# Kernel optimization log

Measured on AMD Instinct MI355X. Metric: run time of the kernel, lower is better.

## Reference

```python
import jax, jax.numpy as jnp
import numpy as np

N_NODES = 50000
N_EDGES = 800000
IN_FEATS = 128
HIDDEN = 128
OUT_LEN = 128


def setup_inputs() -> dict:
    key = jax.random.key(0)
    ks = jax.random.split(key, 8)
    feat = jax.random.normal(ks[0], (N_NODES, IN_FEATS), dtype=jnp.float32)
    # Glorot-ish init for weights, zeros for bias (DGL GraphConv default)
    def w(k, fi, fo):
        return jax.random.normal(k, (fi, fo), dtype=jnp.float32) / np.sqrt(fi)
    W1 = w(ks[1], IN_FEATS, HIDDEN)
    W2 = w(ks[2], HIDDEN, HIDDEN)
    W3 = w(ks[3], HIDDEN, OUT_LEN)
    b1 = jnp.zeros((HIDDEN,), jnp.float32)
    b2 = jnp.zeros((HIDDEN,), jnp.float32)
    b3 = jnp.zeros((OUT_LEN,), jnp.float32)
    src = jax.random.randint(ks[4], (N_EDGES,), 0, N_NODES, dtype=jnp.int32)
    dst = jax.random.randint(ks[5], (N_EDGES,), 0, N_NODES, dtype=jnp.int32)
    return {"feat": feat, "W1": W1, "b1": b1, "W2": W2, "b2": b2,
            "W3": W3, "b3": b3, "src": src, "dst": dst}


def _degree_norm(idx, n):
    # degree counts, clamped to min 1 (DGL behavior), then ^{-1/2}
    deg = jax.ops.segment_sum(jnp.ones_like(idx, dtype=jnp.float32), idx,
                              num_segments=n)
    return jax.lax.rsqrt(jnp.maximum(deg, 1.0))


def _graph_conv(x, W, b, src, dst, out_norm, in_norm):
    # DGL GraphConv, norm='both':
    # h = D_dst^{-1/2} * segsum_dst( D_src^{-1/2} * x[src] ) @ W + b
    h = x * out_norm[:, None]
    m = jax.ops.segment_sum(h[src], dst, num_segments=x.shape[0])  # [N, d]
    m = m * in_norm[:, None]
    return m @ W + b


def reference(feat, W1, b1, W2, b2, W3, b3, src, dst):
    out_norm = _degree_norm(src, feat.shape[0])  # out-degree norm (source)
    in_norm = _degree_norm(dst, feat.shape[0])   # in-degree norm (dest)
    h = jax.nn.relu(_graph_conv(feat, W1, b1, src, dst, out_norm, in_norm))
    h = jax.nn.relu(_graph_conv(h, W2, b2, src, dst, out_norm, in_norm))
    h = _graph_conv(h, W3, b3, src, dst, out_norm, in_norm)
    # single graph: mean_nodes == mean over all nodes, then squeeze -> [out_len]
    return jnp.mean(h, axis=0)
```

## Files before the change

### kernel.cpp

```cpp
#include <hip/hip_runtime.h>

#define N_NODES 50000
#define N_EDGES 800000
#define F 128
#define SCAN_NB 49
#define CH 64
#define EPC (N_EDGES / CH)
#define HALF 25000
#define QTR 12500
#define BSTRIDE 17
#define AGG_NB (N_NODES / 4)
#define RED_NB 256

typedef __bf16 bf16x8 __attribute__((ext_vector_type(8)));
typedef float  f32x4  __attribute__((ext_vector_type(4)));
typedef float  f32x2  __attribute__((ext_vector_type(2)));

__device__ inline unsigned short f2bf(float f) {
    unsigned u = __float_as_uint(f);
    u += 0x7FFF + ((u >> 16) & 1);
    return (unsigned short)(u >> 16);
}
__device__ inline unsigned packbf2(float a, float b) {
    return (unsigned)f2bf(a) | ((unsigned)f2bf(b) << 16);
}

__device__ inline void fp8x8_to_f32(uint2 u, float* f) {
    f32x2 v0 = __builtin_amdgcn_cvt_pk_f32_fp8(u.x, false);
    f32x2 v1 = __builtin_amdgcn_cvt_pk_f32_fp8(u.x, true);
    f32x2 v2 = __builtin_amdgcn_cvt_pk_f32_fp8(u.y, false);
    f32x2 v3 = __builtin_amdgcn_cvt_pk_f32_fp8(u.y, true);
    f[0] = v0.x; f[1] = v0.y; f[2] = v1.x; f[3] = v1.y;
    f[4] = v2.x; f[5] = v2.y; f[6] = v3.x; f[7] = v3.y;
}
__device__ inline unsigned f32x4_to_fp8(float a, float b, float c, float d) {
    unsigned r = __builtin_amdgcn_cvt_pk_fp8_f32(a, b, 0, false);
    r = __builtin_amdgcn_cvt_pk_fp8_f32(c, d, r, true);
    return r;
}

__global__ __launch_bounds__(1024) void hist_kernel(const int* __restrict__ src,
                                                    const int* __restrict__ dst,
                                                    unsigned short* __restrict__ Hs16,
                                                    unsigned short* __restrict__ Hd16) {
    __shared__ unsigned hist[HALF / 2];
    int bx = blockIdx.x;
    int c = bx >> 2, t = bx & 1, h = (bx >> 1) & 1;
    const int* ids = t ? dst : src;
    unsigned short* H = t ? Hd16 : Hs16;
    int base = h * HALF;
    for (int j = threadIdx.x; j < HALF / 2; j += 1024) hist[j] = 0;
    __syncthreads();
    int e0 = c * EPC;
    for (int e = e0 + threadIdx.x; e < e0 + EPC; e += 1024) {
        int id = ids[e] - base;
        if ((unsigned)id < (unsigned)HALF)
            atomicAdd(&hist[id >> 1], 1u << ((id & 1) * 16));
    }
    __syncthreads();
    for (int j = threadIdx.x; j < HALF / 2; j += 1024)
        *(unsigned*)&H[(size_t)c * N_NODES + base + 2 * j] = hist[j];
}

__global__ __launch_bounds__(1024) void reduceN_kernel(const unsigned short* __restrict__ Hs16,
                                                       const unsigned short* __restrict__ Hd16,
                                                       float* __restrict__ onorm,
                                                       float* __restrict__ inorm,
                                                       int* __restrict__ degd,
                                                       int* __restrict__ bsums) {
    __shared__ int wsum[16];
    int i = blockIdx.x * 1024 + threadIdx.x;
    int dd = 0;
    if (i < N_NODES) {
        int ds = 0;
        for (int c = 0; c < CH; c++) {
            ds += Hs16[(size_t)c * N_NODES + i];
            dd += Hd16[(size_t)c * N_NODES + i];
        }
        onorm[i] = rsqrtf(fmaxf((float)ds, 1.0f));
        inorm[i] = rsqrtf(fmaxf((float)dd, 1.0f));
        degd[i] = dd;
    }
    int v = dd;
#pragma unroll
    for (int off = 32; off; off >>= 1) v += __shfl_down(v, off);
    if ((threadIdx.x & 63) == 0) wsum[threadIdx.x >> 6] = v;
    __syncthreads();
    if (threadIdx.x == 0) {
        int s = 0;
#pragma unroll
        for (int k = 0; k < 16; k++) s += wsum[k];
        bsums[blockIdx.x] = s;
    }
}

__global__ __launch_bounds__(64) void scanB_kernel(const int* __restrict__ blockSums,
                                                   int* __restrict__ blockOffs) {
    int t = threadIdx.x;
    int v = (t < SCAN_NB) ? blockSums[t] : 0;
    int incl = v;
#pragma unroll
    for (int off = 1; off < 64; off <<= 1) {
        int u = __shfl_up(incl, off);
        if (t >= off) incl += u;
    }
    if (t < SCAN_NB) blockOffs[t] = incl - v;
}

__global__ __launch_bounds__(1024) void tq_kernel(const int* __restrict__ src,
                                                  const int* __restrict__ dst,
                                                  const float* __restrict__ inorm,
                                                  float* __restrict__ Tq) {
    __shared__ float a[QTR];
    int bx = blockIdx.x;
    int c = bx >> 2, q = bx & 3;
    int base = q * QTR;
    for (int j = threadIdx.x; j < QTR; j += 1024) a[j] = 0.0f;
    __syncthreads();
    int e0 = c * EPC;
    for (int e = e0 + threadIdx.x; e < e0 + EPC; e += 1024) {
        int s = src[e] - base;
        if ((unsigned)s < (unsigned)QTR)
            atomicAdd(&a[s], inorm[dst[e]]);
    }
    __syncthreads();
    for (int j = threadIdx.x; j < QTR; j += 1024)
        Tq[(size_t)c * N_NODES + base + j] = a[j];
}

__global__ __launch_bounds__(1024) void scanC_kernel(const int* __restrict__ deg,
                                                     const int* __restrict__ blockOffs,
                                                     int* __restrict__ rowst,
                                                     const unsigned short* __restrict__ Hd16,
                                                     int* __restrict__ P,
                                                     const float* __restrict__ Tq,
                                                     float* __restrict__ qt) {
    __shared__ int wsum[16];
    int t = threadIdx.x, lane = t & 63, w = t >> 6;
    int i = blockIdx.x * 1024 + t;
    int v = (i < N_NODES) ? deg[i] : 0;
    int incl = v;
#pragma unroll
    for (int off = 1; off < 64; off <<= 1) {
        int u = __shfl_up(incl, off);
        if (lane >= off) incl += u;
    }
    if (lane == 63) wsum[w] = incl;
    __syncthreads();
    if (t == 0) {
        int s = 0;
#pragma unroll
        for (int k = 0; k < 16; k++) { int x = wsum[k]; wsum[k] = s; s += x; }
    }
    __syncthreads();
    incl += wsum[w] + blockOffs[blockIdx.x];
    if (i < N_NODES) {
        int s = incl - v;
        rowst[i] = s;
        if (i == N_NODES - 1) rowst[N_NODES] = incl;
        float tsum = 0.0f;
        for (int c = 0; c < CH; c++) {
            size_t o = (size_t)c * N_NODES + i;
            P[o] = s; s += Hd16[o];
            tsum += Tq[o];
        }
        qt[i] = tsum;
    }
}

__global__ __launch_bounds__(1024) void scatter2_kernel(const int* __restrict__ src,
                                                        const int* __restrict__ dst,
                                                        const int* __restrict__ P,
                                                        int* __restrict__ esrc) {
    __shared__ int cur[QTR];
    int bx = blockIdx.x;
    int c = bx >> 2, q = bx & 3;
    int base = q * QTR;
    for (int j = threadIdx.x; j < QTR; j += 1024)
        cur[j] = P[(size_t)c * N_NODES + base + j];
    __syncthreads();
    int e0 = c * EPC;
    for (int e = e0 + threadIdx.x; e < e0 + EPC; e += 1024) {
        int d = dst[e] - base;
        if ((unsigned)d < (unsigned)QTR) {
            int pos = atomicAdd(&cur[d], 1);
            esrc[pos] = src[e];
        }
    }
}

__global__ __launch_bounds__(256) void cvt_kernel(const float* __restrict__ x,
                                                  const float* __restrict__ onorm,
                                                  uint2* __restrict__ xq, int n8) {
    int i = blockIdx.x * 256 + threadIdx.x;
    if (i < n8) {
        float w = onorm[i >> 4];
        const float4* xv = (const float4*)x;
        float4 v0 = xv[i * 2], v1 = xv[i * 2 + 1];
        uint2 o;
        o.x = f32x4_to_fp8(v0.x * w, v0.y * w, v0.z * w, v0.w * w);
        o.y = f32x4_to_fp8(v1.x * w, v1.y * w, v1.z * w, v1.w * w);
        xq[i] = o;
    }
}

__global__ __launch_bounds__(128) void wprep_kernel(const float* __restrict__ W1,
                                                    const float* __restrict__ W2,
                                                    unsigned short* __restrict__ Wt_hi,
                                                    unsigned short* __restrict__ Wt_lo) {
    int bx = blockIdx.x;
    int wi = bx >> 7, n = bx & 127;
    const float* W = wi ? W2 : W1;
    int k = threadIdx.x;
    float v = W[k * F + n];
    unsigned short hi = f2bf(v);
    float r = v - __uint_as_float((unsigned)hi << 16);
    size_t o = (size_t)wi * F * F + (size_t)n * F + k;
    Wt_hi[o] = hi;
    Wt_lo[o] = f2bf(r);
}

__global__ __launch_bounds__(256) void agg_csr_kernel(const uint2* __restrict__ xq,
                                                      uint4* __restrict__ mb,
                                                      const int* __restrict__ rowst,
                                                      const int* __restrict__ esrc,
                                                      const float* __restrict__ inorm) {
    int w = threadIdx.x >> 6;
    int lane = threadIdx.x & 63;
    int g = lane >> 4, t = lane & 15;
    int row = blockIdx.x * 4 + w;
    int beg = __builtin_amdgcn_readfirstlane(rowst[row]);
    int end = __builtin_amdgcn_readfirstlane(rowst[row + 1]);
    float acc[8];
#pragma unroll
    for (int k = 0; k < 8; k++) acc[k] = 0.0f;

    for (int e = beg; e < end; e += 16) {
        int ea = min(e + g,      end - 1);
        int eb = min(e + 4 + g,  end - 1);
        int ec = min(e + 8 + g,  end - 1);
        int ed = min(e + 12 + g, end - 1);
        int sa = esrc[ea], sb = esrc[eb], sc = esrc[ec], sd = esrc[ed];
        uint2 ua = xq[(size_t)sa * 16 + t];
        uint2 ub = xq[(size_t)sb * 16 + t];
        uint2 uc = xq[(size_t)sc * 16 + t];
        uint2 ud = xq[(size_t)sd * 16 + t];
        float wa = (e + g      < end) ? 1.0f : 0.0f;
        float wb = (e + 4 + g  < end) ? 1.0f : 0.0f;
        float wc = (e + 8 + g  < end) ? 1.0f : 0.0f;
        float wd = (e + 12 + g < end) ? 1.0f : 0.0f;
        float fa[8], fb[8], fc[8], fd[8];
        fp8x8_to_f32(ua, fa); fp8x8_to_f32(ub, fb);
        fp8x8_to_f32(uc, fc); fp8x8_to_f32(ud, fd);
#pragma unroll
        for (int k = 0; k < 8; k++)
            acc[k] += fa[k] * wa + fb[k] * wb + fc[k] * wc + fd[k] * wd;
    }
#pragma unroll
    for (int k = 0; k < 8; k++) {
        acc[k] += __shfl_xor(acc[k], 16, 64);
        acc[k] += __shfl_xor(acc[k], 32, 64);
    }
    if (g == 0) {
        float inw = inorm[row];
        uint4 o;
        o.x = packbf2(acc[0] * inw, acc[1] * inw);
        o.y = packbf2(acc[2] * inw, acc[3] * inw);
        o.z = packbf2(acc[4] * inw, acc[5] * inw);
        o.w = packbf2(acc[6] * inw, acc[7] * inw);
        mb[(size_t)row * 16 + t] = o;
    }
}

__global__ __launch_bounds__(256) void mfma_gemm_kernel(const unsigned short* __restrict__ A,
                                                        const unsigned short* __restrict__ Wt_hi,
                                                        const unsigned short* __restrict__ Wt_lo,
                                                        const float* __restrict__ bias,
                                                        const float* __restrict__ onorm,
                                                        unsigned char* __restrict__ Y8) {
    __shared__ uint4 sB[F * BSTRIDE];
    int tid = threadIdx.x;
    int w = tid >> 6;
    int lane = tid & 63;
    int quad = lane >> 4, r16 = lane & 15;
    int row0 = blockIdx.x * 64 + w * 16;

    const uint4* Arow = (const uint4*)(A + (size_t)(row0 + r16) * F);
    uint4 a[4];
#pragma unroll
    for (int kk = 0; kk < 4; kk++) a[kk] = Arow[kk * 4 + quad];

    f32x4 acc[8];
#pragma unroll
    for (int t = 0; t < 8; t++) acc[t] = (f32x4){0.f, 0.f, 0.f, 0.f};

    const uint4* G[2] = {(const uint4*)Wt_hi, (const uint4*)Wt_lo};
#pragma unroll
    for (int ph = 0; ph < 2; ph++) {
        if (ph) __syncthreads();
        for (int j = tid; j < F * 16; j += 256)
            sB[(j >> 4) * BSTRIDE + (j & 15)] = G[ph][j];
        __syncthreads();
#pragma unroll
        for (int kk = 0; kk < 4; kk++) {
            bf16x8 av = __builtin_bit_cast(bf16x8, a[kk]);
#pragma unroll
            for (int t = 0; t < 8; t++) {
                bf16x8 bv = __builtin_bit_cast(bf16x8,
                    sB[(t * 16 + r16) * BSTRIDE + kk * 4 + quad]);
                acc[t] = __builtin_amdgcn_mfma_f32_16x16x32_bf16(av, bv, acc[t], 0, 0, 0);
            }
        }
    }

    float onw[4];
#pragma unroll
    for (int reg = 0; reg < 4; reg++) {
        int row = row0 + quad * 4 + reg;
        onw[reg] = (row < N_NODES) ? onorm[row] : 0.0f;
    }
#pragma unroll
    for (int t = 0; t < 8; t++) {
        int col = t * 16 + r16;
        float bb = bias[col];
#pragma unroll
        for (int reg = 0; reg < 4; reg++) {
            int row = row0 + quad * 4 + reg;
            if (row < N_NODES) {
                float v = fmaxf(acc[t][reg] + bb, 0.0f) * onw[reg];
                unsigned p = __builtin_amdgcn_cvt_pk_fp8_f32(v, v, 0, false);
                Y8[(size_t)row * F + col] = (unsigned char)(p & 0xFF);
            }
        }
    }
}

__global__ __launch_bounds__(256) void colsum_kernel(const unsigned short* __restrict__ x8,
                                                     const float* __restrict__ qt,
                                                     float* __restrict__ part2) {
    __shared__ float sP[4][F];
    int tid = threadIdx.x;
    int w = tid >> 6, lane = tid & 63;
    float a0 = 0.0f, a1 = 0.0f;
    for (int r = blockIdx.x * 4 + w; r < N_NODES; r += RED_NB * 4) {
        float q = qt[r];
        unsigned us = x8[(size_t)r * 64 + lane];
        f32x2 v = __builtin_amdgcn_cvt_pk_f32_fp8(us, false);
        a0 += v.x * q; a1 += v.y * q;
    }
    sP[w][lane * 2] = a0; sP[w][lane * 2 + 1] = a1;
    __syncthreads();
    if (tid < F)
        part2[(size_t)blockIdx.x * F + tid] =
            sP[0][tid] + sP[1][tid] + sP[2][tid] + sP[3][tid];
}

__global__ __launch_bounds__(1024) void final_kernel(const float* __restrict__ part2,
                                                     const float* __restrict__ W3,
                                                     const float* __restrict__ b3,
                                                     float* __restrict__ out) {
    __shared__ float sc[8][F];
    int tid = threadIdx.x;
    int col = tid & 127, sl = tid >> 7;
    float acc = 0.0f;
    for (int b = sl; b < RED_NB; b += 8) acc += part2[(size_t)b * F + col];
    sc[sl][col] = acc;
    __syncthreads();
    if (tid < F) {
        float s = 0.0f;
#pragma unroll
        for (int k = 0; k < 8; k++) s += sc[k][tid];
        sc[0][tid] = s * (1.0f / (float)N_NODES);
    }
    __syncthreads();
    if (tid < F) {
        float o = b3[tid];
        for (int k = 0; k < F; k++) o += sc[0][k] * W3[k * F + tid];
        out[tid] = o;
    }
}

extern "C" void kernel_launch(void* const* d_in, const int* in_sizes, int n_in,
                              void* d_out, int out_size, void* d_ws, size_t ws_size,
                              hipStream_t stream) {
    const float* feat = (const float*)d_in[0];
    const float* W1   = (const float*)d_in[1];
    const float* b1   = (const float*)d_in[2];
    const float* W2   = (const float*)d_in[3];
    const float* b2   = (const float*)d_in[4];
    const float* W3   = (const float*)d_in[5];
    const float* b3   = (const float*)d_in[6];
    const int*   src  = (const int*)d_in[7];
    const int*   dst  = (const int*)d_in[8];
    float* out = (float*)d_out;

    char* ws = (char*)d_ws;
    size_t off = 0;
    uint4* mb    = (uint4*)(ws + off); off += (size_t)N_NODES * F * 2;
    float* Tq    = (float*)(ws + off); off += (size_t)CH * N_NODES * 4;
    int*   P     = (int*)  (ws + off); off += (size_t)CH * N_NODES * 4;
    unsigned short* Hs16 = (unsigned short*)(ws + off); off += (size_t)CH * N_NODES * 2;
    unsigned short* Hd16 = (unsigned short*)(ws + off); off += (size_t)CH * N_NODES * 2;
    uint2* xq    = (uint2*)(ws + off); off += (size_t)N_NODES * F;
    uint2* hq    = (uint2*)(ws + off); off += (size_t)N_NODES * F;
    unsigned short* Wt_hi = (unsigned short*)(ws + off); off += 2 * F * F * 2;
    unsigned short* Wt_lo = (unsigned short*)(ws + off); off += 2 * F * F * 2;
    float* part2 = (float*)(ws + off); off += (size_t)RED_NB * F * 4;
    int*   esrc  = (int*)  (ws + off); off += (size_t)N_EDGES * 4;
    float* onorm = (float*)(ws + off); off += N_NODES * 4;
    float* inorm = (float*)(ws + off); off += N_NODES * 4;
    float* qt    = (float*)(ws + off); off += N_NODES * 4;
    int*   degd  = (int*)  (ws + off); off += N_NODES * 4;
    int*   rowst = (int*)  (ws + off); off += (N_NODES + 1) * 4;
    int*   bsums = (int*)  (ws + off); off += 64 * 4;
    int*   boffs = (int*)  (ws + off); off += 64 * 4;

    const int GB = (N_NODES + 63) / 64;

    hist_kernel<<<4 * CH, 1024, 0, stream>>>(src, dst, Hs16, Hd16);
    reduceN_kernel<<<SCAN_NB, 1024, 0, stream>>>(Hs16, Hd16, onorm, inorm, degd, bsums);
    scanB_kernel<<<1, 64, 0, stream>>>(bsums, boffs);
    tq_kernel<<<4 * CH, 1024, 0, stream>>>(src, dst, inorm, Tq);
    scanC_kernel<<<SCAN_NB, 1024, 0, stream>>>(degd, boffs, rowst, Hd16, P, Tq, qt);
    scatter2_kernel<<<4 * CH, 1024, 0, stream>>>(src, dst, P, esrc);

    cvt_kernel<<<(N_NODES * F / 8 + 255) / 256, 256, 0, stream>>>(feat, onorm, xq, N_NODES * F / 8);
    wprep_kernel<<<256, 128, 0, stream>>>(W1, W2, Wt_hi, Wt_lo);

    agg_csr_kernel<<<AGG_NB, 256, 0, stream>>>(xq, mb, rowst, esrc, inorm);
    mfma_gemm_kernel<<<GB, 256, 0, stream>>>((const unsigned short*)mb, Wt_hi, Wt_lo, b1,
                                             onorm, (unsigned char*)hq);
    agg_csr_kernel<<<AGG_NB, 256, 0, stream>>>(hq, mb, rowst, esrc, inorm);
    mfma_gemm_kernel<<<GB, 256, 0, stream>>>((const unsigned short*)mb, Wt_hi + F * F,
                                             Wt_lo + F * F, b2, onorm, (unsigned char*)xq);
    colsum_kernel<<<RED_NB, 256, 0, stream>>>((const unsigned short*)xq, qt, part2);
    final_kernel<<<1, 1024, 0, stream>>>(part2, W3, b3, out);
}
```

Baseline: 245.9 us.

## Merge graph-build stages and epilogue into cooperative kernels with grid syncs

Eight preprocessing launches (histogram, degree reduce, block scan, Tq, row-start scan, scatter, feature conversion, weight prep) are replaced by one cooperative kernel. The stages are now separated by grid.sync, and the small block-offset scan is folded into a serial prefix sum in each block. The colsum and final kernels are likewise merged into one cooperative kernel. This removes launch gaps and inter-kernel bubbles. In exchange it adds grid-wide barrier costs and requires all 256 blocks of 1024 threads with 50KB of shared memory to be co-resident, and the conversion and weight-prep loops now run on fewer threads.

Result: slower. 442.8 us (+80.1%).

```diff
diff --git a/kernel.cpp b/kernel.cpp
--- a/kernel.cpp
+++ b/kernel.cpp
@@ -1,4 +1,7 @@
 #include <hip/hip_runtime.h>
+#include <hip/hip_cooperative_groups.h>
+
+namespace cg = cooperative_groups;
 
 #define N_NODES 50000
 #define N_EDGES 800000
@@ -39,185 +42,162 @@
     return r;
 }
 
-__global__ __launch_bounds__(1024) void hist_kernel(const int* __restrict__ src,
-                                                    const int* __restrict__ dst,
-                                                    unsigned short* __restrict__ Hs16,
-                                                    unsigned short* __restrict__ Hd16) {
-    __shared__ unsigned hist[HALF / 2];
-    int bx = blockIdx.x;
-    int c = bx >> 2, t = bx & 1, h = (bx >> 1) & 1;
-    const int* ids = t ? dst : src;
-    unsigned short* H = t ? Hd16 : Hs16;
-    int base = h * HALF;
-    for (int j = threadIdx.x; j < HALF / 2; j += 1024) hist[j] = 0;
-    __syncthreads();
-    int e0 = c * EPC;
-    for (int e = e0 + threadIdx.x; e < e0 + EPC; e += 1024) {
-        int id = ids[e] - base;
-        if ((unsigned)id < (unsigned)HALF)
-            atomicAdd(&hist[id >> 1], 1u << ((id & 1) * 16));
-    }
-    __syncthreads();
-    for (int j = threadIdx.x; j < HALF / 2; j += 1024)
-        *(unsigned*)&H[(size_t)c * N_NODES + base + 2 * j] = hist[j];
-}
-
-__global__ __launch_bounds__(1024) void reduceN_kernel(const unsigned short* __restrict__ Hs16,
-                                                       const unsigned short* __restrict__ Hd16,
-                                                       float* __restrict__ onorm,
-                                                       float* __restrict__ inorm,
-                                                       int* __restrict__ degd,
-                                                       int* __restrict__ bsums) {
-    __shared__ int wsum[16];
-    int i = blockIdx.x * 1024 + threadIdx.x;
-    int dd = 0;
-    if (i < N_NODES) {
-        int ds = 0;
-        for (int c = 0; c < CH; c++) {
-            ds += Hs16[(size_t)c * N_NODES + i];
-            dd += Hd16[(size_t)c * N_NODES + i];
-        }
-        onorm[i] = rsqrtf(fmaxf((float)ds, 1.0f));
-        inorm[i] = rsqrtf(fmaxf((float)dd, 1.0f));
-        degd[i] = dd;
-    }
-    int v = dd;
-#pragma unroll
-    for (int off = 32; off; off >>= 1) v += __shfl_down(v, off);
-    if ((threadIdx.x & 63) == 0) wsum[threadIdx.x >> 6] = v;
-    __syncthreads();
-    if (threadIdx.x == 0) {
-        int s = 0;
-#pragma unroll
-        for (int k = 0; k < 16; k++) s += wsum[k];
-        bsums[blockIdx.x] = s;
-    }
-}
-
-__global__ __launch_bounds__(64) void scanB_kernel(const int* __restrict__ blockSums,
-                                                   int* __restrict__ blockOffs) {
-    int t = threadIdx.x;
-    int v = (t < SCAN_NB) ? blockSums[t] : 0;
-    int incl = v;
-#pragma unroll
-    for (int off = 1; off < 64; off <<= 1) {
-        int u = __shfl_up(incl, off);
-        if (t >= off) incl += u;
-    }
-    if (t < SCAN_NB) blockOffs[t] = incl - v;
-}
-
-__global__ __launch_bounds__(1024) void tq_kernel(const int* __restrict__ src,
-                                                  const int* __restrict__ dst,
-                                                  const float* __restrict__ inorm,
-                                                  float* __restrict__ Tq) {
-    __shared__ float a[QTR];
-    int bx = blockIdx.x;
-    int c = bx >> 2, q = bx & 3;
-    int base = q * QTR;
-    for (int j = threadIdx.x; j < QTR; j += 1024) a[j] = 0.0f;
-    __syncthreads();
-    int e0 = c * EPC;
-    for (int e = e0 + threadIdx.x; e < e0 + EPC; e += 1024) {
-        int s = src[e] - base;
-        if ((unsigned)s < (unsigned)QTR)
-            atomicAdd(&a[s], inorm[dst[e]]);
-    }
-    __syncthreads();
-    for (int j = threadIdx.x; j < QTR; j += 1024)
-        Tq[(size_t)c * N_NODES + base + j] = a[j];
-}
-
-__global__ __launch_bounds__(1024) void scanC_kernel(const int* __restrict__ deg,
-                                                     const int* __restrict__ blockOffs,
-                                                     int* __restrict__ rowst,
-                                                     const unsigned short* __restrict__ Hd16,
-                                                     int* __restrict__ P,
-                                                     const float* __restrict__ Tq,
-                                                     float* __restrict__ qt) {
-    __shared__ int wsum[16];
-    int t = threadIdx.x, lane = t & 63, w = t >> 6;
-    int i = blockIdx.x * 1024 + t;
-    int v = (i < N_NODES) ? deg[i] : 0;
-    int incl = v;
-#pragma unroll
-    for (int off = 1; off < 64; off <<= 1) {
-        int u = __shfl_up(incl, off);
-        if (lane >= off) incl += u;
-    }
-    if (lane == 63) wsum[w] = incl;
-    __syncthreads();
-    if (t == 0) {
-        int s = 0;
-#pragma unroll
-        for (int k = 0; k < 16; k++) { int x = wsum[k]; wsum[k] = s; s += x; }
-    }
-    __syncthreads();
-    incl += wsum[w] + blockOffs[blockIdx.x];
-    if (i < N_NODES) {
-        int s = incl - v;
-        rowst[i] = s;
-        if (i == N_NODES - 1) rowst[N_NODES] = incl;
-        float tsum = 0.0f;
-        for (int c = 0; c < CH; c++) {
-            size_t o = (size_t)c * N_NODES + i;
-            P[o] = s; s += Hd16[o];
-            tsum += Tq[o];
-        }
-        qt[i] = tsum;
-    }
-}
-
-__global__ __launch_bounds__(1024) void scatter2_kernel(const int* __restrict__ src,
-                                                        const int* __restrict__ dst,
-                                                        const int* __restrict__ P,
-                                                        int* __restrict__ esrc) {
-    __shared__ int cur[QTR];
-    int bx = blockIdx.x;
-    int c = bx >> 2, q = bx & 3;
-    int base = q * QTR;
-    for (int j = threadIdx.x; j < QTR; j += 1024)
-        cur[j] = P[(size_t)c * N_NODES + base + j];
-    __syncthreads();
-    int e0 = c * EPC;
-    for (int e = e0 + threadIdx.x; e < e0 + EPC; e += 1024) {
-        int d = dst[e] - base;
-        if ((unsigned)d < (unsigned)QTR) {
-            int pos = atomicAdd(&cur[d], 1);
-            esrc[pos] = src[e];
-        }
-    }
-}
-
-__global__ __launch_bounds__(256) void cvt_kernel(const float* __restrict__ x,
-                                                  const float* __restrict__ onorm,
-                                                  uint2* __restrict__ xq, int n8) {
-    int i = blockIdx.x * 256 + threadIdx.x;
-    if (i < n8) {
-        float w = onorm[i >> 4];
-        const float4* xv = (const float4*)x;
+__global__ __launch_bounds__(1024) void build_kernel(
+        const int* __restrict__ src, const int* __restrict__ dst,
+        unsigned short* __restrict__ Hs16, unsigned short* __restrict__ Hd16,
+        float* __restrict__ onorm, float* __restrict__ inorm,
+        int* __restrict__ degd, int* __restrict__ bsums,
+        int* __restrict__ rowst, int* __restrict__ P,
+        float* __restrict__ Tq, float* __restrict__ qt,
+        int* __restrict__ esrc,
+        const float* __restrict__ feat, uint2* __restrict__ xq,
+        const float* __restrict__ W1, const float* __restrict__ W2,
+        unsigned short* __restrict__ Wt_hi, unsigned short* __restrict__ Wt_lo) {
+    cg::grid_group grid = cg::this_grid();
+    __shared__ unsigned sh[QTR];
+    int bx = blockIdx.x, tid = threadIdx.x;
+
+    {
+        int c = bx >> 2, ty = bx & 1, h = (bx >> 1) & 1;
+        const int* ids = ty ? dst : src;
+        unsigned short* H = ty ? Hd16 : Hs16;
+        int base = h * HALF;
+        for (int j = tid; j < HALF / 2; j += 1024) sh[j] = 0;
+        __syncthreads();
+        int e0 = c * EPC;
+        for (int e = e0 + tid; e < e0 + EPC; e += 1024) {
+            int id = ids[e] - base;
+            if ((unsigned)id < (unsigned)HALF)
+                atomicAdd(&sh[id >> 1], 1u << ((id & 1) * 16));
+        }
+        __syncthreads();
+        for (int j = tid; j < HALF / 2; j += 1024)
+            *(unsigned*)&H[(size_t)c * N_NODES + base + 2 * j] = sh[j];
+    }
+    grid.sync();
+
+    if (bx < SCAN_NB) {
+        int* wsum = (int*)sh;
+        int i = bx * 1024 + tid;
+        int dd = 0;
+        if (i < N_NODES) {
+            int ds = 0;
+            for (int c = 0; c < CH; c++) {
+                ds += Hs16[(size_t)c * N_NODES + i];
+                dd += Hd16[(size_t)c * N_NODES + i];
+            }
+            onorm[i] = rsqrtf(fmaxf((float)ds, 1.0f));
+            inorm[i] = rsqrtf(fmaxf((float)dd, 1.0f));
+            degd[i] = dd;
+        }
+        int v = dd;
+#pragma unroll
+        for (int off = 32; off; off >>= 1) v += __shfl_down(v, off);
+        if ((tid & 63) == 0) wsum[tid >> 6] = v;
+        __syncthreads();
+        if (tid == 0) {
+            int s = 0;
+#pragma unroll
+            for (int k = 0; k < 16; k++) s += wsum[k];
+            bsums[bx] = s;
+        }
+    }
+    grid.sync();
+
+    {
+        float* a = (float*)sh;
+        int c = bx >> 2, q = bx & 3;
+        int base = q * QTR;
+        for (int j = tid; j < QTR; j += 1024) a[j] = 0.0f;
+        __syncthreads();
+        int e0 = c * EPC;
+        for (int e = e0 + tid; e < e0 + EPC; e += 1024) {
+            int s = src[e] - base;
+            if ((unsigned)s < (unsigned)QTR)
+                atomicAdd(&a[s], inorm[dst[e]]);
+        }
+        __syncthreads();
+        for (int j = tid; j < QTR; j += 1024)
+            Tq[(size_t)c * N_NODES + base + j] = a[j];
+    }
+    grid.sync();
+
+    if (bx < SCAN_NB) {
+        int* wsum = (int*)sh;
+        int lane = tid & 63, w = tid >> 6;
+        int i = bx * 1024 + tid;
+        int v = (i < N_NODES) ? degd[i] : 0;
+        int incl = v;
+#pragma unroll
+        for (int off = 1; off < 64; off <<= 1) {
+            int u = __shfl_up(incl, off);
+            if (lane >= off) incl += u;
+        }
+        if (lane == 63) wsum[w] = incl;
+        __syncthreads();
+        if (tid == 0) {
+            int boff = 0;
+            for (int k = 0; k < bx; k++) boff += bsums[k];
+            int s = boff;
+#pragma unroll
+            for (int k = 0; k < 16; k++) { int x = wsum[k]; wsum[k] = s; s += x; }
+        }
+        __syncthreads();
+        incl += wsum[w];
+        if (i < N_NODES) {
+            int s = incl - v;
+            rowst[i] = s;
+            if (i == N_NODES - 1) rowst[N_NODES] = incl;
+            float tsum = 0.0f;
+            for (int c = 0; c < CH; c++) {
+                size_t o = (size_t)c * N_NODES + i;
+                P[o] = s; s += Hd16[o];
+                tsum += Tq[o];
+            }
+            qt[i] = tsum;
+        }
+    }
+    grid.sync();
+
+    {
+        int* cur = (int*)sh;
+        int c = bx >> 2, q = bx & 3;
+        int base = q * QTR;
+        for (int j = tid; j < QTR; j += 1024)
+            cur[j] = P[(size_t)c * N_NODES + base + j];
+        __syncthreads();
+        int e0 = c * EPC;
+        for (int e = e0 + tid; e < e0 + EPC; e += 1024) {
+            int d = dst[e] - base;
+            if ((unsigned)d < (unsigned)QTR) {
+                int pos = atomicAdd(&cur[d], 1);
+                esrc[pos] = src[e];
+            }
+        }
+    }
+
+    int T = gridDim.x * 1024;
+    int id0 = bx * 1024 + tid;
+    for (int i = id0; i < N_NODES * F / 8; i += T) {
+        float wgt = onorm[i >> 4];
+        const float4* xv = (const float4*)feat;
         float4 v0 = xv[i * 2], v1 = xv[i * 2 + 1];
         uint2 o;
-        o.x = f32x4_to_fp8(v0.x * w, v0.y * w, v0.z * w, v0.w * w);
-        o.y = f32x4_to_fp8(v1.x * w, v1.y * w, v1.z * w, v1.w * w);
+        o.x = f32x4_to_fp8(v0.x * wgt, v0.y * wgt, v0.z * wgt, v0.w * wgt);
+        o.y = f32x4_to_fp8(v1.x * wgt, v1.y * wgt, v1.z * wgt, v1.w * wgt);
         xq[i] = o;
     }
-}
-
-__global__ __launch_bounds__(128) void wprep_kernel(const float* __restrict__ W1,
-                                                    const float* __restrict__ W2,
-                                                    unsigned short* __restrict__ Wt_hi,
-                                                    unsigned short* __restrict__ Wt_lo) {
-    int bx = blockIdx.x;
-    int wi = bx >> 7, n = bx & 127;
-    const float* W = wi ? W2 : W1;
-    int k = threadIdx.x;
-    float v = W[k * F + n];
-    unsigned short hi = f2bf(v);
-    float r = v - __uint_as_float((unsigned)hi << 16);
-    size_t o = (size_t)wi * F * F + (size_t)n * F + k;
-    Wt_hi[o] = hi;
-    Wt_lo[o] = f2bf(r);
+    for (int i = id0; i < 2 * F * F; i += T) {
+        int wi = i >> 14, rem = i & 16383;
+        int n = rem >> 7, k = rem & 127;
+        const float* W = wi ? W2 : W1;
+        float v = W[k * F + n];
+        unsigned short hi = f2bf(v);
+        float r = v - __uint_as_float((unsigned)hi << 16);
+        size_t o = (size_t)wi * F * F + (size_t)n * F + k;
+        Wt_hi[o] = hi;
+        Wt_lo[o] = f2bf(r);
+    }
 }
 
 __global__ __launch_bounds__(256) void agg_csr_kernel(const uint2* __restrict__ xq,
@@ -335,12 +315,19 @@
     }
 }
 
-__global__ __launch_bounds__(256) void colsum_kernel(const unsigned short* __restrict__ x8,
-                                                     const float* __restrict__ qt,
-                                                     float* __restrict__ part2) {
+__global__ __launch_bounds__(256) void epi_kernel(const unsigned short* __restrict__ x8,
+                                                  const float* __restrict__ qt,
+                                                  float* __restrict__ part2,
+                                                  const float* __restrict__ W3,
+                                                  const float* __restrict__ b3,
+                                                  float* __restrict__ out) {
+    cg::grid_group grid = cg::this_grid();
     __shared__ float sP[4][F];
+    __shared__ float sc2[2][F];
+    __shared__ float cvec[F];
     int tid = threadIdx.x;
     int w = tid >> 6, lane = tid & 63;
+
     float a0 = 0.0f, a1 = 0.0f;
     for (int r = blockIdx.x * 4 + w; r < N_NODES; r += RED_NB * 4) {
         float q = qt[r];
@@ -353,30 +340,21 @@
     if (tid < F)
         part2[(size_t)blockIdx.x * F + tid] =
             sP[0][tid] + sP[1][tid] + sP[2][tid] + sP[3][tid];
-}
-
-__global__ __launch_bounds__(1024) void final_kernel(const float* __restrict__ part2,
-                                                     const float* __restrict__ W3,
-                                                     const float* __restrict__ b3,
-                                                     float* __restrict__ out) {
-    __shared__ float sc[8][F];
-    int tid = threadIdx.x;
-    int col = tid & 127, sl = tid >> 7;
-    float acc = 0.0f;
-    for (int b = sl; b < RED_NB; b += 8) acc += part2[(size_t)b * F + col];
-    sc[sl][col] = acc;
-    __syncthreads();
-    if (tid < F) {
-        float s = 0.0f;
-#pragma unroll
-        for (int k = 0; k < 8; k++) s += sc[k][tid];
-        sc[0][tid] = s * (1.0f / (float)N_NODES);
-    }
-    __syncthreads();
-    if (tid < F) {
-        float o = b3[tid];
-        for (int k = 0; k < F; k++) o += sc[0][k] * W3[k * F + tid];
-        out[tid] = o;
+    grid.sync();
+
+    if (blockIdx.x == 0) {
+        int sl = tid >> 7, col = tid & 127;
+        float acc = 0.0f;
+        for (int b = sl; b < RED_NB; b += 2) acc += part2[(size_t)b * F + col];
+        sc2[sl][col] = acc;
+        __syncthreads();
+        if (tid < F) cvec[tid] = (sc2[0][tid] + sc2[1][tid]) * (1.0f / (float)N_NODES);
+        __syncthreads();
+        if (tid < F) {
+            float o = b3[tid];
+            for (int k = 0; k < F; k++) o += cvec[k] * W3[k * F + tid];
+            out[tid] = o;
+        }
     }
 }
 
@@ -413,19 +391,18 @@
     int*   degd  = (int*)  (ws + off); off += N_NODES * 4;
     int*   rowst = (int*)  (ws + off); off += (N_NODES + 1) * 4;
     int*   bsums = (int*)  (ws + off); off += 64 * 4;
-    int*   boffs = (int*)  (ws + off); off += 64 * 4;
 
     const int GB = (N_NODES + 63) / 64;
 
-    hist_kernel<<<4 * CH, 1024, 0, stream>>>(src, dst, Hs16, Hd16);
-    reduceN_kernel<<<SCAN_NB, 1024, 0, stream>>>(Hs16, Hd16, onorm, inorm, degd, bsums);
-    scanB_kernel<<<1, 64, 0, stream>>>(bsums, boffs);
-    tq_kernel<<<4 * CH, 1024, 0, stream>>>(src, dst, inorm, Tq);
-    scanC_kernel<<<SCAN_NB, 1024, 0, stream>>>(degd, boffs, rowst, Hd16, P, Tq, qt);
-    scatter2_kernel<<<4 * CH, 1024, 0, stream>>>(src, dst, P, esrc);
-
-    cvt_kernel<<<(N_NODES * F / 8 + 255) / 256, 256, 0, stream>>>(feat, onorm, xq, N_NODES * F / 8);
-    wprep_kernel<<<256, 128, 0, stream>>>(W1, W2, Wt_hi, Wt_lo);
+    {
+        void* args[] = {(void*)&src, (void*)&dst, (void*)&Hs16, (void*)&Hd16,
+                        (void*)&onorm, (void*)&inorm, (void*)&degd, (void*)&bsums,
+                        (void*)&rowst, (void*)&P, (void*)&Tq, (void*)&qt,
+                        (void*)&esrc, (void*)&feat, (void*)&xq,
+                        (void*)&W1, (void*)&W2, (void*)&Wt_hi, (void*)&Wt_lo};
+        hipLaunchCooperativeKernel((void*)build_kernel, dim3(4 * CH), dim3(1024),
+                                   args, 0, stream);
+    }
 
     agg_csr_kernel<<<AGG_NB, 256, 0, stream>>>(xq, mb, rowst, esrc, inorm);
     mfma_gemm_kernel<<<GB, 256, 0, stream>>>((const unsigned short*)mb, Wt_hi, Wt_lo, b1,
@@ -433,6 +410,12 @@
     agg_csr_kernel<<<AGG_NB, 256, 0, stream>>>(hq, mb, rowst, esrc, inorm);
     mfma_gemm_kernel<<<GB, 256, 0, stream>>>((const unsigned short*)mb, Wt_hi + F * F,
                                              Wt_lo + F * F, b2, onorm, (unsigned char*)xq);
-    colsum_kernel<<<RED_NB, 256, 0, stream>>>((const unsigned short*)xq, qt, part2);
-    final_kernel<<<1, 1024, 0, stream>>>(part2, W3, b3, out);
-}
+
+    {
+        const unsigned short* x8 = (const unsigned short*)xq;
+        void* args[] = {(void*)&x8, (void*)&qt, (void*)&part2,
+                        (void*)&W3, (void*)&b3, (void*)&out};
+        hipLaunchCooperativeKernel((void*)epi_kernel, dim3(RED_NB), dim3(256),
+                                   args, 0, stream);
+    }
+}
```

## Fold scan, cast and weight-prep kernels into neighbors; fuse colsum into final GEMM

Applied to the files above, without the earlier changes.

Removes the scanB, cvt, wprep and colsum launches. Their work moves into reduceN, which now also does the fp8 feature cast and the weight hi/lo split. scanC computes its block offset serially from bsums, and the second GEMM does the qt-weighted column reduction in its epilogue instead of writing fp8 activations and reading them back. This cuts launch overhead and a full fp8 write/read round trip. In exchange, the fp8 cast runs on only about 49 blocks with a per-thread strided row walk, which gives poor coalescing and low parallelism. Reducing in full precision before quantization also changes numerics slightly.

Result: slower. 272.4 us (+10.8%).

```diff
diff --git a/kernel.cpp b/kernel.cpp
--- a/kernel.cpp
+++ b/kernel.cpp
@@ -10,7 +10,7 @@
 #define QTR 12500
 #define BSTRIDE 17
 #define AGG_NB (N_NODES / 4)
-#define RED_NB 256
+#define GB ((N_NODES + 63) / 64)
 
 typedef __bf16 bf16x8 __attribute__((ext_vector_type(8)));
 typedef float  f32x4  __attribute__((ext_vector_type(4)));
@@ -67,17 +67,25 @@
                                                        float* __restrict__ onorm,
                                                        float* __restrict__ inorm,
                                                        int* __restrict__ degd,
-                                                       int* __restrict__ bsums) {
+                                                       int* __restrict__ bsums,
+                                                       const float* __restrict__ feat,
+                                                       uint2* __restrict__ xq,
+                                                       const float* __restrict__ W1,
+                                                       const float* __restrict__ W2,
+                                                       unsigned short* __restrict__ Wt_hi,
+                                                       unsigned short* __restrict__ Wt_lo) {
     __shared__ int wsum[16];
     int i = blockIdx.x * 1024 + threadIdx.x;
     int dd = 0;
+    float onw = 0.0f;
     if (i < N_NODES) {
         int ds = 0;
         for (int c = 0; c < CH; c++) {
             ds += Hs16[(size_t)c * N_NODES + i];
             dd += Hd16[(size_t)c * N_NODES + i];
         }
-        onorm[i] = rsqrtf(fmaxf((float)ds, 1.0f));
+        onw = rsqrtf(fmaxf((float)ds, 1.0f));
+        onorm[i] = onw;
         inorm[i] = rsqrtf(fmaxf((float)dd, 1.0f));
         degd[i] = dd;
     }
@@ -92,19 +100,30 @@
         for (int k = 0; k < 16; k++) s += wsum[k];
         bsums[blockIdx.x] = s;
     }
-}
-
-__global__ __launch_bounds__(64) void scanB_kernel(const int* __restrict__ blockSums,
-                                                   int* __restrict__ blockOffs) {
-    int t = threadIdx.x;
-    int v = (t < SCAN_NB) ? blockSums[t] : 0;
-    int incl = v;
-#pragma unroll
-    for (int off = 1; off < 64; off <<= 1) {
-        int u = __shfl_up(incl, off);
-        if (t >= off) incl += u;
-    }
-    if (t < SCAN_NB) blockOffs[t] = incl - v;
+    if (i < N_NODES) {
+        const float4* fv = (const float4*)feat + (size_t)i * 32;
+        uint2* xo = xq + (size_t)i * 16;
+#pragma unroll 4
+        for (int k = 0; k < 16; k++) {
+            float4 v0 = fv[2 * k], v1 = fv[2 * k + 1];
+            uint2 o;
+            o.x = f32x4_to_fp8(v0.x * onw, v0.y * onw, v0.z * onw, v0.w * onw);
+            o.y = f32x4_to_fp8(v1.x * onw, v1.y * onw, v1.z * onw, v1.w * onw);
+            xo[k] = o;
+        }
+    }
+    int id0 = blockIdx.x * 1024 + threadIdx.x;
+    if (id0 < 2 * F * F) {
+        int wi = id0 >> 14, rem = id0 & 16383;
+        int n = rem >> 7, k = rem & 127;
+        const float* W = wi ? W2 : W1;
+        float v2 = W[k * F + n];
+        unsigned short hi = f2bf(v2);
+        float r = v2 - __uint_as_float((unsigned)hi << 16);
+        size_t o = (size_t)wi * F * F + (size_t)n * F + k;
+        Wt_hi[o] = hi;
+        Wt_lo[o] = f2bf(r);
+    }
 }
 
 __global__ __launch_bounds__(1024) void tq_kernel(const int* __restrict__ src,
@@ -129,7 +148,7 @@
 }
 
 __global__ __launch_bounds__(1024) void scanC_kernel(const int* __restrict__ deg,
-                                                     const int* __restrict__ blockOffs,
+                                                     const int* __restrict__ bsums,
                                                      int* __restrict__ rowst,
                                                      const unsigned short* __restrict__ Hd16,
                                                      int* __restrict__ P,
@@ -149,11 +168,12 @@
     __syncthreads();
     if (t == 0) {
         int s = 0;
+        for (int k = 0; k < (int)blockIdx.x; k++) s += bsums[k];
 #pragma unroll
         for (int k = 0; k < 16; k++) { int x = wsum[k]; wsum[k] = s; s += x; }
     }
     __syncthreads();
-    incl += wsum[w] + blockOffs[blockIdx.x];
+    incl += wsum[w];
     if (i < N_NODES) {
         int s = incl - v;
         rowst[i] = s;
@@ -187,37 +207,6 @@
             esrc[pos] = src[e];
         }
     }
-}
-
-__global__ __launch_bounds__(256) void cvt_kernel(const float* __restrict__ x,
-                                                  const float* __restrict__ onorm,
-                                                  uint2* __restrict__ xq, int n8) {
-    int i = blockIdx.x * 256 + threadIdx.x;
-    if (i < n8) {
-        float w = onorm[i >> 4];
-        const float4* xv = (const float4*)x;
-        float4 v0 = xv[i * 2], v1 = xv[i * 2 + 1];
-        uint2 o;
-        o.x = f32x4_to_fp8(v0.x * w, v0.y * w, v0.z * w, v0.w * w);
-        o.y = f32x4_to_fp8(v1.x * w, v1.y * w, v1.z * w, v1.w * w);
-        xq[i] = o;
-    }
-}
-
-__global__ __launch_bounds__(128) void wprep_kernel(const float* __restrict__ W1,
-                                                    const float* __restrict__ W2,
-                                                    unsigned short* __restrict__ Wt_hi,
-                                                    unsigned short* __restrict__ Wt_lo) {
-    int bx = blockIdx.x;
-    int wi = bx >> 7, n = bx & 127;
-    const float* W = wi ? W2 : W1;
-    int k = threadIdx.x;
-    float v = W[k * F + n];
-    unsigned short hi = f2bf(v);
-    float r = v - __uint_as_float((unsigned)hi << 16);
-    size_t o = (size_t)wi * F * F + (size_t)n * F + k;
-    Wt_hi[o] = hi;
-    Wt_lo[o] = f2bf(r);
 }
 
 __global__ __launch_bounds__(256) void agg_csr_kernel(const uint2* __restrict__ xq,
@@ -272,13 +261,17 @@
     }
 }
 
+template <int FINAL>
 __global__ __launch_bounds__(256) void mfma_gemm_kernel(const unsigned short* __restrict__ A,
                                                         const unsigned short* __restrict__ Wt_hi,
                                                         const unsigned short* __restrict__ Wt_lo,
                                                         const float* __restrict__ bias,
                                                         const float* __restrict__ onorm,
-                                                        unsigned char* __restrict__ Y8) {
+                                                        unsigned char* __restrict__ Y8,
+                                                        const float* __restrict__ qt,
+                                                        float* __restrict__ part2) {
     __shared__ uint4 sB[F * BSTRIDE];
+    __shared__ float sPf[4][F];
     int tid = threadIdx.x;
     int w = tid >> 6;
     int lane = tid & 63;
@@ -313,46 +306,46 @@
         }
     }
 
-    float onw[4];
+    float rw[4];
 #pragma unroll
     for (int reg = 0; reg < 4; reg++) {
         int row = row0 + quad * 4 + reg;
-        onw[reg] = (row < N_NODES) ? onorm[row] : 0.0f;
-    }
-#pragma unroll
-    for (int t = 0; t < 8; t++) {
-        int col = t * 16 + r16;
-        float bb = bias[col];
-#pragma unroll
-        for (int reg = 0; reg < 4; reg++) {
-            int row = row0 + quad * 4 + reg;
-            if (row < N_NODES) {
-                float v = fmaxf(acc[t][reg] + bb, 0.0f) * onw[reg];
-                unsigned p = __builtin_amdgcn_cvt_pk_fp8_f32(v, v, 0, false);
-                Y8[(size_t)row * F + col] = (unsigned char)(p & 0xFF);
+        rw[reg] = (row < N_NODES) ? (FINAL ? qt[row] * onorm[row] : onorm[row]) : 0.0f;
+    }
+
+    if (!FINAL) {
+#pragma unroll
+        for (int t = 0; t < 8; t++) {
+            int col = t * 16 + r16;
+            float bb = bias[col];
+#pragma unroll
+            for (int reg = 0; reg < 4; reg++) {
+                int row = row0 + quad * 4 + reg;
+                if (row < N_NODES) {
+                    float v = fmaxf(acc[t][reg] + bb, 0.0f) * rw[reg];
+                    unsigned p = __builtin_amdgcn_cvt_pk_fp8_f32(v, v, 0, false);
+                    Y8[(size_t)row * F + col] = (unsigned char)(p & 0xFF);
+                }
             }
         }
-    }
-}
-
-__global__ __launch_bounds__(256) void colsum_kernel(const unsigned short* __restrict__ x8,
-                                                     const float* __restrict__ qt,
-                                                     float* __restrict__ part2) {
-    __shared__ float sP[4][F];
-    int tid = threadIdx.x;
-    int w = tid >> 6, lane = tid & 63;
-    float a0 = 0.0f, a1 = 0.0f;
-    for (int r = blockIdx.x * 4 + w; r < N_NODES; r += RED_NB * 4) {
-        float q = qt[r];
-        unsigned us = x8[(size_t)r * 64 + lane];
-        f32x2 v = __builtin_amdgcn_cvt_pk_f32_fp8(us, false);
-        a0 += v.x * q; a1 += v.y * q;
-    }
-    sP[w][lane * 2] = a0; sP[w][lane * 2 + 1] = a1;
-    __syncthreads();
-    if (tid < F)
-        part2[(size_t)blockIdx.x * F + tid] =
-            sP[0][tid] + sP[1][tid] + sP[2][tid] + sP[3][tid];
+    } else {
+#pragma unroll
+        for (int t = 0; t < 8; t++) {
+            int col = t * 16 + r16;
+            float bb = bias[col];
+            float p = 0.0f;
+#pragma unroll
+            for (int reg = 0; reg < 4; reg++)
+                p += fmaxf(acc[t][reg] + bb, 0.0f) * rw[reg];
+            p += __shfl_xor(p, 16, 64);
+            p += __shfl_xor(p, 32, 64);
+            if (quad == 0) sPf[w][col] = p;
+        }
+        __syncthreads();
+        if (tid < F)
+            part2[(size_t)blockIdx.x * F + tid] =
+                sPf[0][tid] + sPf[1][tid] + sPf[2][tid] + sPf[3][tid];
+    }
 }
 
 __global__ __launch_bounds__(1024) void final_kernel(const float* __restrict__ part2,
@@ -363,7 +356,7 @@
     int tid = threadIdx.x;
     int col = tid & 127, sl = tid >> 7;
     float acc = 0.0f;
-    for (int b = sl; b < RED_NB; b += 8) acc += part2[(size_t)b * F + col];
+    for (int b = sl; b < GB; b += 8) acc += part2[(size_t)b * F + col];
     sc[sl][col] = acc;
     __syncthreads();
     if (tid < F) {
@@ -405,7 +398,7 @@
     uint2* hq    = (uint2*)(ws + off); off += (size_t)N_NODES * F;
     unsigned short* Wt_hi = (unsigned short*)(ws + off); off += 2 * F * F * 2;
     unsigned short* Wt_lo = (unsigned short*)(ws + off); off += 2 * F * F * 2;
-    float* part2 = (float*)(ws + off); off += (size_t)RED_NB * F * 4;
+    float* part2 = (float*)(ws + off); off += (size_t)GB * F * 4;
     int*   esrc  = (int*)  (ws + off); off += (size_t)N_EDGES * 4;
     float* onorm = (float*)(ws + off); off += N_NODES * 4;
     float* inorm = (float*)(ws + off); off += N_NODES * 4;
@@ -413,26 +406,20 @@
     int*   degd  = (int*)  (ws + off); off += N_NODES * 4;
     int*   rowst = (int*)  (ws + off); off += (N_NODES + 1) * 4;
     int*   bsums = (int*)  (ws + off); off += 64 * 4;
-    int*   boffs = (int*)  (ws + off); off += 64 * 4;
-
-    const int GB = (N_NODES + 63) / 64;
 
     hist_kernel<<<4 * CH, 1024, 0, stream>>>(src, dst, Hs16, Hd16);
-    reduceN_kernel<<<SCAN_NB, 1024, 0, stream>>>(Hs16, Hd16, onorm, inorm, degd, bsums);
-    scanB_kernel<<<1, 64, 0, stream>>>(bsums, boffs);
+    reduceN_kernel<<<SCAN_NB, 1024, 0, stream>>>(Hs16, Hd16, onorm, inorm, degd, bsums,
+                                                 feat, xq, W1, W2, Wt_hi, Wt_lo);
     tq_kernel<<<4 * CH, 1024, 0, stream>>>(src, dst, inorm, Tq);
-    scanC_kernel<<<SCAN_NB, 1024, 0, stream>>>(degd, boffs, rowst, Hd16, P, Tq, qt);
+    scanC_kernel<<<SCAN_NB, 1024, 0, stream>>>(degd, bsums, rowst, Hd16, P, Tq, qt);
     scatter2_kernel<<<4 * CH, 1024, 0, stream>>>(src, dst, P, esrc);
 
-    cvt_kernel<<<(N_NODES * F / 8 + 255) / 256, 256, 0, stream>>>(feat, onorm, xq, N_NODES * F / 8);
-    wprep_kernel<<<256, 128, 0, stream>>>(W1, W2, Wt_hi, Wt_lo);
-
     agg_csr_kernel<<<AGG_NB, 256, 0, stream>>>(xq, mb, rowst, esrc, inorm);
-    mfma_gemm_kernel<<<GB, 256, 0, stream>>>((const unsigned short*)mb, Wt_hi, Wt_lo, b1,
-                                             onorm, (unsigned char*)hq);
+    mfma_gemm_kernel<0><<<GB, 256, 0, stream>>>((const unsigned short*)mb, Wt_hi, Wt_lo, b1,
+                                                onorm, (unsigned char*)hq, qt, part2);
     agg_csr_kernel<<<AGG_NB, 256, 0, stream>>>(hq, mb, rowst, esrc, inorm);
-    mfma_gemm_kernel<<<GB, 256, 0, stream>>>((const unsigned short*)mb, Wt_hi + F * F,
-                                             Wt_lo + F * F, b2, onorm, (unsigned char*)xq);
-    colsum_kernel<<<RED_NB, 256, 0, stream>>>((const unsigned short*)xq, qt, part2);
+    mfma_gemm_kernel<1><<<GB, 256, 0, stream>>>((const unsigned short*)mb, Wt_hi + F * F,
+                                                Wt_lo + F * F, b2, onorm,
+                                                (unsigned char*)hq, qt, part2);
     final_kernel<<<1, 1024, 0, stream>>>(part2, W3, b3, out);
 }
```
